# Optimization experiments

Hardware: AMD Instinct MI355X
Metric: run time of the kernel (lower is better)

The kernel has to match this reference:

```python
import jax, jax.numpy as jnp
import numpy as np

B, S, D = 4, 2048, 1024

def setup_inputs() -> dict:
    key = jax.random.key(0)
    ks = jax.random.split(key, 9)
    q = jax.random.normal(ks[0], (B, S, D), dtype=jnp.float32)
    k = jax.random.normal(ks[1], (B, S, D), dtype=jnp.float32)
    v = jax.random.normal(ks[2], (B, S, D), dtype=jnp.float32)
    # Dense layer params (Glorot-ish scale), bias included like keras Dense
    sc = 1.0 / np.sqrt(D)
    Wq = jax.random.normal(ks[3], (D, D), dtype=jnp.float32) * sc
    Wk = jax.random.normal(ks[4], (D, D), dtype=jnp.float32) * sc
    Wv = jax.random.normal(ks[5], (D, D), dtype=jnp.float32) * sc
    bq = jnp.zeros((D,), dtype=jnp.float32)
    bk = jnp.zeros((D,), dtype=jnp.float32)
    bv = jnp.zeros((D,), dtype=jnp.float32)
    # causal mask: 1 where attention is forbidden (future positions)
    mask = jnp.triu(jnp.ones((S, S), dtype=jnp.float32), k=1)
    return {"q": q, "k": k, "v": v, "mask": mask,
            "Wq": Wq, "bq": bq, "Wk": Wk, "bk": bk, "Wv": Wv, "bv": bv}

def reference(q, k, v, mask, Wq, bq, Wk, bk, Wv, bv):
    WQ = q @ Wq + bq                      # [B,S,D]
    WK = k @ Wk + bk
    WV = v @ Wv + bv
    d_k = jnp.asarray(WK.shape[-1], dtype=jnp.float32)
    scores = jnp.einsum('bqd,bkd->bqk', WQ, WK) / jnp.sqrt(d_k)  # [B,S,S]
    scores = scores + mask * (-1e9)
    attn = jax.nn.softmax(scores, axis=-1)
    return jnp.einsum('bqk,bkd->bqd', attn, WV)
```

## Files before the change

kernel.cpp:

```cpp
#include <hip/hip_runtime.h>
#include <math.h>

#define S_LEN 2048
#define D_DIM 1024
#define NB    4

typedef __bf16 bf16_t;
typedef __bf16 bf16x8 __attribute__((ext_vector_type(8)));
typedef float  f32x4  __attribute__((ext_vector_type(4)));

#define BM 128
#define BN 128
#define BK 32

__device__ __forceinline__ void async16(const void* g, void* l) {
    __builtin_amdgcn_global_load_lds(
        (__attribute__((address_space(1))) const void*)g,
        (__attribute__((address_space(3))) void*)l, 16, 0, 0);
}

__device__ __forceinline__ void gemm_bt_core(
    const bf16_t* __restrict__ A, const bf16_t* __restrict__ Bt,
    int lda, int ldb, int m0, int n0, int kTiles, f32x4 (&acc)[4][4])
{
    __shared__ bf16_t lA[BM * BK];
    __shared__ bf16_t lB[BN * BK];
    const int t    = threadIdx.x;
    const int w    = t >> 6;
    const int lane = t & 63;
    const int wr   = w >> 1, wc = w & 1;
    const int srow = lane >> 2;
    const int skk  = (lane & 3) * 8;
    const int fr   = lane & 15, fq = lane >> 4;
    const bf16_t* paBase = lA + (wr * 64 + fr) * BK + fq * 8;
    const bf16_t* pbBase = lB + (wc * 64 + fr) * BK + fq * 8;
    bf16_t* ldsA0 = lA + w * 512;
    bf16_t* ldsA1 = lA + 2048 + w * 512;
    bf16_t* ldsB0 = lB + w * 512;
    bf16_t* ldsB1 = lB + 2048 + w * 512;
    const bf16_t* gA = A  + (long)(m0 + w * 16 + srow) * lda + skk;
    const bf16_t* gB = Bt + (long)(n0 + w * 16 + srow) * ldb + skk;

#pragma unroll
    for (int mt = 0; mt < 4; ++mt)
#pragma unroll
        for (int nt = 0; nt < 4; ++nt)
            acc[mt][nt] = f32x4{0.f, 0.f, 0.f, 0.f};

    for (int kt = 0; kt < kTiles; ++kt) {
        const int k0 = kt * BK;
        async16(gA + k0,             ldsA0);
        async16(gA + k0 + 64L * lda, ldsA1);
        async16(gB + k0,             ldsB0);
        async16(gB + k0 + 64L * ldb, ldsB1);
        asm volatile("s_waitcnt vmcnt(0)" ::: "memory");
        __syncthreads();
        bf16x8 af[4], bfv[4];
#pragma unroll
        for (int mt = 0; mt < 4; ++mt)
            af[mt] = *(const bf16x8*)(paBase + mt * 16 * BK);
#pragma unroll
        for (int nt = 0; nt < 4; ++nt)
            bfv[nt] = *(const bf16x8*)(pbBase + nt * 16 * BK);
#pragma unroll
        for (int mt = 0; mt < 4; ++mt)
#pragma unroll
            for (int nt = 0; nt < 4; ++nt)
                acc[mt][nt] = __builtin_amdgcn_mfma_f32_16x16x32_bf16(
                    af[mt], bfv[nt], acc[mt][nt], 0, 0, 0);
        __syncthreads();
    }
}

__global__ __launch_bounds__(256) void k_f2b(
    const float* __restrict__ q, const float* __restrict__ k,
    const float* __restrict__ v, bf16_t* __restrict__ Xb)
{
    const int z = blockIdx.z;
    const float* src = (z == 0) ? q : ((z == 1) ? k : v);
    bf16_t* dst = Xb + (long)z * ((long)NB * S_LEN * D_DIM);
    const long i = (long)blockIdx.x * blockDim.x + threadIdx.x;
    const float4* s4 = (const float4*)src;
    float4 a = s4[2 * i], c = s4[2 * i + 1];
    bf16x8 o;
    o[0] = (bf16_t)a.x; o[1] = (bf16_t)a.y; o[2] = (bf16_t)a.z; o[3] = (bf16_t)a.w;
    o[4] = (bf16_t)c.x; o[5] = (bf16_t)c.y; o[6] = (bf16_t)c.z; o[7] = (bf16_t)c.w;
    *(bf16x8*)(dst + i * 8) = o;
}

__global__ __launch_bounds__(256) void k_tw(
    const float* __restrict__ Wq, const float* __restrict__ Wk,
    const float* __restrict__ Wv, bf16_t* __restrict__ Wt)
{
    __shared__ float tile[32][33];
    const int z = blockIdx.z;
    const float* W = (z == 0) ? Wq : ((z == 1) ? Wk : Wv);
    bf16_t* T = Wt + (long)z * D_DIM * D_DIM;
    const int tx = threadIdx.x, ty = threadIdx.y;
    const int x  = blockIdx.x * 32 + tx;
    const int y0 = blockIdx.y * 32;
#pragma unroll
    for (int j = ty; j < 32; j += 8) tile[j][tx] = W[(long)(y0 + j) * D_DIM + x];
    __syncthreads();
    const int x2 = blockIdx.y * 32 + tx;
    const int y2 = blockIdx.x * 32;
#pragma unroll
    for (int j = ty; j < 32; j += 8)
        T[(long)(y2 + j) * D_DIM + x2] = (bf16_t)tile[tx][j];
}

__global__ __launch_bounds__(256) void k_tv(
    const bf16_t* __restrict__ PrV, bf16_t* __restrict__ WVt)
{
    __shared__ bf16_t tile[32][33];
    const int b = blockIdx.z;
    const bf16_t* src = PrV + (long)b * S_LEN * D_DIM;
    bf16_t* dst = WVt + (long)b * D_DIM * S_LEN;
    const int tx = threadIdx.x, ty = threadIdx.y;
    const int x  = blockIdx.x * 32 + tx;
    const int y0 = blockIdx.y * 32;
#pragma unroll
    for (int j = ty; j < 32; j += 8) tile[j][tx] = src[(long)(y0 + j) * D_DIM + x];
    __syncthreads();
    const int x2 = blockIdx.y * 32 + tx;
    const int y2 = blockIdx.x * 32;
#pragma unroll
    for (int j = ty; j < 32; j += 8)
        dst[(long)(y2 + j) * S_LEN + x2] = tile[tx][j];
}

__global__ __launch_bounds__(256) void k_gemm_proj(
    const bf16_t* __restrict__ Xb, const bf16_t* __restrict__ Wt,
    const float* __restrict__ bq, const float* __restrict__ bk,
    const float* __restrict__ bv, bf16_t* __restrict__ Pr)
{
    const int z = blockIdx.z;
    const bf16_t* A  = Xb + (long)z * ((long)NB * S_LEN * D_DIM);
    const bf16_t* Bt = Wt + (long)z * D_DIM * D_DIM;
    bf16_t* C        = Pr + (long)z * ((long)NB * S_LEN * D_DIM);
    const float* bias = (z == 0) ? bq : ((z == 1) ? bk : bv);
    const int m0 = blockIdx.x * BM, n0 = blockIdx.y * BN;
    f32x4 acc[4][4];
    gemm_bt_core(A, Bt, D_DIM, D_DIM, m0, n0, D_DIM / BK, acc);
    const int lane = threadIdx.x & 63, w = threadIdx.x >> 6;
    const int wr = w >> 1, wc = w & 1;
    const int r0 = m0 + wr * 64 + (lane >> 4) * 4;
    const int c0 = n0 + wc * 64 + (lane & 15);
#pragma unroll
    for (int mt = 0; mt < 4; ++mt)
#pragma unroll
        for (int nt = 0; nt < 4; ++nt) {
            const int col = c0 + nt * 16;
            const float bb = bias[col];
#pragma unroll
            for (int r = 0; r < 4; ++r) {
                const int row = r0 + mt * 16 + r;
                C[(long)row * D_DIM + col] = (bf16_t)(acc[mt][nt][r] + bb);
            }
        }
}

__global__ __launch_bounds__(256) void k_gemm_scores(
    const bf16_t* __restrict__ PrQ, const bf16_t* __restrict__ PrK,
    bf16_t* __restrict__ SC)
{
    const int ti = blockIdx.y, tj = blockIdx.x, b = blockIdx.z;
    if (tj > ti) return;
    const bf16_t* A  = PrQ + (long)b * S_LEN * D_DIM;
    const bf16_t* Bt = PrK + (long)b * S_LEN * D_DIM;
    bf16_t* C        = SC  + (long)b * S_LEN * S_LEN;
    const int m0 = ti * BM, n0 = tj * BN;
    f32x4 acc[4][4];
    gemm_bt_core(A, Bt, D_DIM, D_DIM, m0, n0, D_DIM / BK, acc);
    const int lane = threadIdx.x & 63, w = threadIdx.x >> 6;
    const int wr = w >> 1, wc = w & 1;
    const int r0 = m0 + wr * 64 + (lane >> 4) * 4;
    const int c0 = n0 + wc * 64 + (lane & 15);
#pragma unroll
    for (int mt = 0; mt < 4; ++mt)
#pragma unroll
        for (int nt = 0; nt < 4; ++nt) {
            const int col = c0 + nt * 16;
#pragma unroll
            for (int r = 0; r < 4; ++r) {
                const int row = r0 + mt * 16 + r;
                C[(long)row * S_LEN + col] = (bf16_t)(acc[mt][nt][r] * 0.03125f);
            }
        }
}

__global__ __launch_bounds__(256) void k_softmax(bf16_t* __restrict__ SC)
{
    __shared__ float buf[S_LEN];
    __shared__ float red[256];
    const int i = blockIdx.x, b = blockIdx.y;
    bf16_t* row = SC + ((long)b * S_LEN + i) * S_LEN;
    const int n = i + 1;
    const int t = threadIdx.x;
    float mx = -3.4e38f;
    for (int j = t; j < n; j += 256) { float x = (float)row[j]; buf[j] = x; mx = fmaxf(mx, x); }
    red[t] = mx; __syncthreads();
    for (int s = 128; s > 0; s >>= 1) { if (t < s) red[t] = fmaxf(red[t], red[t + s]); __syncthreads(); }
    const float M = red[0];
    __syncthreads();
    float sm = 0.f;
    for (int j = t; j < n; j += 256) { float e = __expf(buf[j] - M); buf[j] = e; sm += e; }
    red[t] = sm; __syncthreads();
    for (int s = 128; s > 0; s >>= 1) { if (t < s) red[t] += red[t + s]; __syncthreads(); }
    const float inv = 1.0f / red[0];
    for (int j = t; j < n; j += 256) row[j] = (bf16_t)(buf[j] * inv);
    const int jend = ((i >> 7) + 1) << 7;
    for (int j = n + t; j < jend; j += 256) row[j] = (bf16_t)0.f;
}

__global__ __launch_bounds__(256) void k_gemm_pv(
    const bf16_t* __restrict__ SC, const bf16_t* __restrict__ WVt,
    float* __restrict__ Out)
{
    const int ti = blockIdx.y, b = blockIdx.z;
    const bf16_t* A  = SC  + (long)b * S_LEN * S_LEN;
    const bf16_t* Bt = WVt + (long)b * D_DIM * S_LEN;
    float* C         = Out + (long)b * S_LEN * D_DIM;
    const int m0 = ti * BM, n0 = blockIdx.x * BN;
    f32x4 acc[4][4];
    gemm_bt_core(A, Bt, S_LEN, S_LEN, m0, n0, (ti + 1) * (BM / BK), acc);
    const int lane = threadIdx.x & 63, w = threadIdx.x >> 6;
    const int wr = w >> 1, wc = w & 1;
    const int r0 = m0 + wr * 64 + (lane >> 4) * 4;
    const int c0 = n0 + wc * 64 + (lane & 15);
#pragma unroll
    for (int mt = 0; mt < 4; ++mt)
#pragma unroll
        for (int nt = 0; nt < 4; ++nt) {
            const int col = c0 + nt * 16;
#pragma unroll
            for (int r = 0; r < 4; ++r) {
                const int row = r0 + mt * 16 + r;
                C[(long)row * D_DIM + col] = acc[mt][nt][r];
            }
        }
}

extern "C" void kernel_launch(void* const* d_in, const int* in_sizes, int n_in,
                              void* d_out, int out_size, void* d_ws, size_t ws_size,
                              hipStream_t stream)
{
    (void)in_sizes; (void)n_in; (void)out_size; (void)ws_size;
    const float* q  = (const float*)d_in[0];
    const float* k  = (const float*)d_in[1];
    const float* v  = (const float*)d_in[2];
    const float* Wq = (const float*)d_in[4];
    const float* bq = (const float*)d_in[5];
    const float* Wk = (const float*)d_in[6];
    const float* bk = (const float*)d_in[7];
    const float* Wv = (const float*)d_in[8];
    const float* bv = (const float*)d_in[9];
    float* out = (float*)d_out;

    bf16_t* ws = (bf16_t*)d_ws;
    const long nW = (long)D_DIM * D_DIM;
    const long nX = (long)NB * S_LEN * D_DIM;
    bf16_t* Wt  = ws;
    bf16_t* Xb  = Wt + 3 * nW;
    bf16_t* SC  = Xb;
    bf16_t* Pr  = Xb + 3 * nX;
    bf16_t* WVt = Pr + 3 * nX;
    bf16_t* PrQ = Pr;
    bf16_t* PrK = Pr + nX;
    bf16_t* PrV = Pr + 2 * nX;

    k_f2b        <<<dim3(4096, 1, 3),  256,        0, stream>>>(q, k, v, Xb);
    k_tw         <<<dim3(32, 32, 3),   dim3(32,8), 0, stream>>>(Wq, Wk, Wv, Wt);
    k_gemm_proj  <<<dim3(64, 8, 3),    256,        0, stream>>>(Xb, Wt, bq, bk, bv, Pr);
    k_tv         <<<dim3(32, 64, NB),  dim3(32,8), 0, stream>>>(PrV, WVt);
    k_gemm_scores<<<dim3(16, 16, NB),  256,        0, stream>>>(PrQ, PrK, SC);
    k_softmax    <<<dim3(S_LEN, NB),   256,        0, stream>>>(SC);
    k_gemm_pv    <<<dim3(8, 16, NB),   256,        0, stream>>>(SC, WVt, out);
}
```

Before: 363.0 us.

## Swizzle GEMM LDS layout, warp-per-row softmax, and reverse PV tile order

```diff
diff --git a/kernel.cpp b/kernel.cpp
--- a/kernel.cpp
+++ b/kernel.cpp
@@ -30,10 +30,11 @@
     const int lane = t & 63;
     const int wr   = w >> 1, wc = w & 1;
     const int srow = lane >> 2;
-    const int skk  = (lane & 3) * 8;
+    const int skk  = (((lane & 3) ^ ((lane >> 3) & 3)) * 8);
     const int fr   = lane & 15, fq = lane >> 4;
-    const bf16_t* paBase = lA + (wr * 64 + fr) * BK + fq * 8;
-    const bf16_t* pbBase = lB + (wc * 64 + fr) * BK + fq * 8;
+    const int fof  = (fq ^ ((fr >> 1) & 3)) * 8;
+    const bf16_t* paBase = lA + (wr * 64 + fr) * BK + fof;
+    const bf16_t* pbBase = lB + (wc * 64 + fr) * BK + fof;
     bf16_t* ldsA0 = lA + w * 512;
     bf16_t* ldsA1 = lA + 2048 + w * 512;
     bf16_t* ldsB0 = lB + w * 512;
@@ -191,33 +192,62 @@
 
 __global__ __launch_bounds__(256) void k_softmax(bf16_t* __restrict__ SC)
 {
-    __shared__ float buf[S_LEN];
-    __shared__ float red[256];
-    const int i = blockIdx.x, b = blockIdx.y;
+    const int w = threadIdx.x >> 6, lane = threadIdx.x & 63;
+    const int i = blockIdx.x * 4 + w;
+    const int b = blockIdx.y;
     bf16_t* row = SC + ((long)b * S_LEN + i) * S_LEN;
-    const int n = i + 1;
-    const int t = threadIdx.x;
-    float mx = -3.4e38f;
-    for (int j = t; j < n; j += 256) { float x = (float)row[j]; buf[j] = x; mx = fmaxf(mx, x); }
-    red[t] = mx; __syncthreads();
-    for (int s = 128; s > 0; s >>= 1) { if (t < s) red[t] = fmaxf(red[t], red[t + s]); __syncthreads(); }
-    const float M = red[0];
-    __syncthreads();
+    const int n    = i + 1;
+    const int jend = ((i >> 7) + 1) << 7;
+    const int nch  = (jend + 511) >> 9;
+    float x[4][8];
+    float mx = -1e30f;
+#pragma unroll
+    for (int c = 0; c < 4; ++c) {
+        if (c < nch) {
+            bf16x8 vv = *(const bf16x8*)(row + c * 512 + lane * 8);
+#pragma unroll
+            for (int e = 0; e < 8; ++e) {
+                const int j = c * 512 + lane * 8 + e;
+                const float f = (j < n) ? (float)vv[e] : -1e30f;
+                x[c][e] = f;
+                mx = fmaxf(mx, f);
+            }
+        }
+    }
+#pragma unroll
+    for (int d = 1; d < 64; d <<= 1) mx = fmaxf(mx, __shfl_xor(mx, d, 64));
     float sm = 0.f;
-    for (int j = t; j < n; j += 256) { float e = __expf(buf[j] - M); buf[j] = e; sm += e; }
-    red[t] = sm; __syncthreads();
-    for (int s = 128; s > 0; s >>= 1) { if (t < s) red[t] += red[t + s]; __syncthreads(); }
-    const float inv = 1.0f / red[0];
-    for (int j = t; j < n; j += 256) row[j] = (bf16_t)(buf[j] * inv);
-    const int jend = ((i >> 7) + 1) << 7;
-    for (int j = n + t; j < jend; j += 256) row[j] = (bf16_t)0.f;
+#pragma unroll
+    for (int c = 0; c < 4; ++c) {
+        if (c < nch) {
+#pragma unroll
+            for (int e = 0; e < 8; ++e) {
+                const int j = c * 512 + lane * 8 + e;
+                float p = (j < n) ? __expf(x[c][e] - mx) : 0.f;
+                x[c][e] = p;
+                sm += p;
+            }
+        }
+    }
+#pragma unroll
+    for (int d = 1; d < 64; d <<= 1) sm += __shfl_xor(sm, d, 64);
+    const float inv = 1.0f / sm;
+#pragma unroll
+    for (int c = 0; c < 4; ++c) {
+        if (c < nch) {
+            bf16x8 o;
+#pragma unroll
+            for (int e = 0; e < 8; ++e) o[e] = (bf16_t)(x[c][e] * inv);
+            *(bf16x8*)(row + c * 512 + lane * 8) = o;
+        }
+    }
 }
 
 __global__ __launch_bounds__(256) void k_gemm_pv(
     const bf16_t* __restrict__ SC, const bf16_t* __restrict__ WVt,
     float* __restrict__ Out)
 {
-    const int ti = blockIdx.y, b = blockIdx.z;
+    const int ti = (S_LEN / BM - 1) - blockIdx.y, b = blockIdx.z;
     const bf16_t* A  = SC  + (long)b * S_LEN * S_LEN;
     const bf16_t* Bt = WVt + (long)b * D_DIM * S_LEN;
     float* C         = Out + (long)b * S_LEN * D_DIM;
@@ -269,11 +299,11 @@
     bf16_t* PrK = Pr + nX;
     bf16_t* PrV = Pr + 2 * nX;
 
-    k_f2b        <<<dim3(4096, 1, 3),  256,        0, stream>>>(q, k, v, Xb);
-    k_tw         <<<dim3(32, 32, 3),   dim3(32,8), 0, stream>>>(Wq, Wk, Wv, Wt);
-    k_gemm_proj  <<<dim3(64, 8, 3),    256,        0, stream>>>(Xb, Wt, bq, bk, bv, Pr);
-    k_tv         <<<dim3(32, 64, NB),  dim3(32,8), 0, stream>>>(PrV, WVt);
-    k_gemm_scores<<<dim3(16, 16, NB),  256,        0, stream>>>(PrQ, PrK, SC);
-    k_softmax    <<<dim3(S_LEN, NB),   256,        0, stream>>>(SC);
-    k_gemm_pv    <<<dim3(8, 16, NB),   256,        0, stream>>>(SC, WVt, out);
-}
+    k_f2b        <<<dim3(4096, 1, 3),   256,        0, stream>>>(q, k, v, Xb);
+    k_tw         <<<dim3(32, 32, 3),    dim3(32,8), 0, stream>>>(Wq, Wk, Wv, Wt);
+    k_gemm_proj  <<<dim3(64, 8, 3),     256,        0, stream>>>(Xb, Wt, bq, bk, bv, Pr);
+    k_tv         <<<dim3(32, 64, NB),   dim3(32,8), 0, stream>>>(PrV, WVt);
+    k_gemm_scores<<<dim3(16, 16, NB),   256,        0, stream>>>(PrQ, PrK, SC);
+    k_softmax    <<<dim3(S_LEN / 4, NB),256,        0, stream>>>(SC);
+    k_gemm_pv    <<<dim3(8, 16, NB),    256,        0, stream>>>(SC, WVt, out);
+}
```

After: 349.4 us. 1.04x faster.
